# Performance work log

Hardware: AMD Instinct MI355X
Metric: run time of the kernel (lower is better)

The kernel has to match this reference:

```python
import jax, jax.numpy as jnp
import numpy as np

E, K = 16, 4          # n_experts, top_k
C, H = 2048, 3584     # d_model, ffn_hidden
B, T = 2, 512
STD = 0.02


def setup_inputs() -> dict:
    key = jax.random.key(0)
    ks = jax.random.split(key, 5)
    x = jax.random.normal(ks[0], (B, T, C), jnp.float32)
    W_up = jax.random.normal(ks[1], (E, H, C), jnp.float32) * STD
    W_gate = jax.random.normal(ks[2], (E, H, C), jnp.float32) * STD
    W_down = jax.random.normal(ks[3], (E, C, H), jnp.float32) * STD
    gate_inp = jax.random.normal(ks[4], (E, C), jnp.float32) * STD
    return {"x": x, "W_up": W_up, "W_gate": W_gate, "W_down": W_down,
            "gate_inp": gate_inp}


def reference(x, W_up, W_gate, W_down, gate_inp):
    # x: [B, T, C]
    b, t, c = x.shape
    xf = x.reshape(b * t, c)                                  # [N, C]
    logits = xf @ gate_inp.T                                  # [N, E]
    topv, topi = jax.lax.top_k(logits, K)                     # [N, K]
    w = jax.nn.softmax(topv.astype(jnp.float32), axis=-1).astype(x.dtype)
    n = xf.shape[0]
    # Dense combine weights: zero for unselected experts -> identical math
    # to the original per-token gather, without the [N,K,H,C] blowup.
    dense_w = jnp.zeros((n, E), x.dtype).at[jnp.arange(n)[:, None], topi].set(w)
    u = jnp.einsum('nc,ehc->neh', xf, W_up)                   # [N, E, H]
    g = jnp.einsum('nc,ehc->neh', xf, W_gate)                 # [N, E, H]
    h = jax.nn.silu(g) * u                                    # SwiGLU
    y = jnp.einsum('neh,ech,ne->nc', h, W_down, dense_w)      # weighted combine
    return y.reshape(b, t, c)
```

## Files before the change

kernel.cpp:

```cpp
#include <hip/hip_runtime.h>
#include <math.h>

#define NTOK   1024
#define EXP    16
#define TOPK   4
#define DMODEL 2048
#define DFFN   3584
#define HT_TILES 56
#define CT_TILES 32

typedef __attribute__((ext_vector_type(8))) short bf16x8;
typedef __attribute__((ext_vector_type(4))) float f32x4;

#define O_COUNTS 0
#define O_BASE   256
#define O_CURSOR 512
#define O_TOPI   4096
#define O_TOPW   (O_TOPI + 16384)
#define O_TOK    (O_TOPW + 16384)
#define O_WGT    (O_TOK + 16384)
#define O_SLOTNK (O_WGT + 16384)
#define O_HBUF   (O_SLOTNK + 16384)
#define O_YPART  (O_HBUF + (size_t)4096*DFFN*2)

__device__ __forceinline__ unsigned short f2b_rne(float f) {
  unsigned u = __builtin_bit_cast(unsigned, f);
  u += 0x7FFFu + ((u >> 16) & 1u);
  return (unsigned short)(u >> 16);
}
__device__ __forceinline__ float b2f(unsigned short h) {
  unsigned u = ((unsigned)h) << 16;
  return __builtin_bit_cast(float, u);
}

__device__ __forceinline__ void st_bf16x4(unsigned short* lds, int row, int c4, float4 v) {
  unsigned long long p = (unsigned long long)f2b_rne(v.x)
    | ((unsigned long long)f2b_rne(v.y) << 16)
    | ((unsigned long long)f2b_rne(v.z) << 32)
    | ((unsigned long long)f2b_rne(v.w) << 48);
  *(unsigned long long*)(lds + row*64 + (((c4 >> 1) ^ (row & 7)) * 8) + (c4 & 1) * 4) = p;
}
__device__ __forceinline__ bf16x8 ld_frag(const unsigned short* lds, int row, int chunk) {
  return *(const bf16x8*)(lds + row*64 + ((chunk ^ (row & 7)) * 8));
}

__global__ void k_zero(int* counts, int* cursor) {
  int t = threadIdx.x;
  if (t < EXP) { counts[t] = 0; cursor[t] = 0; }
}

__global__ void k_gate(const float* __restrict__ x, const float* __restrict__ gi,
                       int* __restrict__ topi, float* __restrict__ topw,
                       int* __restrict__ counts) {
  int n = blockIdx.x;
  int lane = threadIdx.x & 63, wave = threadIdx.x >> 6;
  __shared__ float lg[EXP];
  const float4* xr = (const float4*)(x + (size_t)n * DMODEL);
  #pragma unroll
  for (int i = 0; i < 4; ++i) {
    int e = wave * 4 + i;
    const float4* gr = (const float4*)(gi + (size_t)e * DMODEL);
    float s = 0.f;
    #pragma unroll
    for (int j = 0; j < 8; ++j) {
      float4 a = xr[j*64 + lane];
      float4 b = gr[j*64 + lane];
      s += a.x*b.x + a.y*b.y + a.z*b.z + a.w*b.w;
    }
    #pragma unroll
    for (int off = 32; off; off >>= 1) s += __shfl_xor(s, off);
    if (lane == 0) lg[e] = s;
  }
  __syncthreads();
  if (threadIdx.x == 0) {
    float v[EXP];
    #pragma unroll
    for (int j = 0; j < EXP; ++j) v[j] = lg[j];
    int bi[TOPK]; float bv[TOPK];
    #pragma unroll
    for (int k = 0; k < TOPK; ++k) {
      float best = -3.4e38f; int bidx = 0;
      for (int j = 0; j < EXP; ++j) if (v[j] > best) { best = v[j]; bidx = j; }
      bv[k] = best; bi[k] = bidx; v[bidx] = -3.4e38f;
    }
    float m = bv[0], ss = 0.f, w[TOPK];
    #pragma unroll
    for (int k = 0; k < TOPK; ++k) { w[k] = expf(bv[k] - m); ss += w[k]; }
    #pragma unroll
    for (int k = 0; k < TOPK; ++k) {
      topi[n*TOPK + k] = bi[k];
      topw[n*TOPK + k] = w[k] / ss;
      atomicAdd(&counts[bi[k]], 1);
    }
  }
}

__global__ void k_prefix(const int* __restrict__ counts, int* __restrict__ basep) {
  if (threadIdx.x == 0) {
    int acc = 0;
    for (int e = 0; e < EXP; ++e) { basep[e] = acc; acc += counts[e]; }
  }
}

__global__ void k_scatter(const int* __restrict__ topi, const float* __restrict__ topw,
                          const int* __restrict__ basep, int* __restrict__ cursor,
                          int* __restrict__ tok, float* __restrict__ wgt,
                          int* __restrict__ slotnk) {
  int n = blockIdx.x * blockDim.x + threadIdx.x;
  if (n >= NTOK) return;
  #pragma unroll
  for (int k = 0; k < TOPK; ++k) {
    int e = topi[n*TOPK + k];
    int pos = atomicAdd(&cursor[e], 1);
    int slot = basep[e] + pos;
    tok[slot] = n;
    wgt[slot] = topw[n*TOPK + k];
    slotnk[n*TOPK + k] = slot;
  }
}

__global__ __launch_bounds__(256) void k_upgate(
    const float* __restrict__ x, const float* __restrict__ Wu, const float* __restrict__ Wg,
    const int* __restrict__ counts, const int* __restrict__ basep,
    const int* __restrict__ tok, const float* __restrict__ wgt,
    unsigned short* __restrict__ hbuf) {
  int e  = blockIdx.x / HT_TILES;
  int ht = blockIdx.x % HT_TILES;
  int n_e = counts[e];
  if (n_e == 0) return;
  int base_e = basep[e];
  int nm = (n_e + 127) >> 7;

  __shared__ unsigned short xs[128*64];
  __shared__ unsigned short us[64*64];
  __shared__ unsigned short gs[64*64];
  __shared__ int   stok[128];
  __shared__ float swgt[128];

  int tid = threadIdx.x;
  int lane = tid & 63, wave = tid >> 6;
  int wm = wave >> 1, wh = wave & 1;
  const float* wu_base = Wu + ((size_t)e * DFFN + (size_t)ht * 64) * DMODEL;
  const float* wg_base = Wg + ((size_t)e * DFFN + (size_t)ht * 64) * DMODEL;

  for (int mch = 0; mch < nm; ++mch) {
    __syncthreads();
    if (tid < 128) {
      int r = mch*128 + tid;
      bool valid = r < n_e;
      stok[tid] = valid ? tok[base_e + r] : 0;
      swgt[tid] = valid ? wgt[base_e + r] : 0.f;
    }
    f32x4 ua[4][2], ga[4][2];
    #pragma unroll
    for (int t = 0; t < 4; ++t)
      #pragma unroll
      for (int j = 0; j < 2; ++j) {
        f32x4 z = {0.f, 0.f, 0.f, 0.f};
        ua[t][j] = z; ga[t][j] = z;
      }

    for (int kc = 0; kc < DMODEL/64; ++kc) {
      __syncthreads();
      #pragma unroll
      for (int i = 0; i < 8; ++i) {
        int idx = i*256 + tid;
        int row = idx >> 4, c4 = idx & 15;
        float4 v = *(const float4*)(x + (size_t)stok[row]*DMODEL + kc*64 + c4*4);
        st_bf16x4(xs, row, c4, v);
      }
      #pragma unroll
      for (int i = 0; i < 4; ++i) {
        int idx = i*256 + tid;
        int row = idx >> 4, c4 = idx & 15;
        st_bf16x4(us, row, c4, *(const float4*)(wu_base + (size_t)row*DMODEL + kc*64 + c4*4));
        st_bf16x4(gs, row, c4, *(const float4*)(wg_base + (size_t)row*DMODEL + kc*64 + c4*4));
      }
      __syncthreads();
      #pragma unroll
      for (int kk = 0; kk < 2; ++kk) {
        int chunk = kk*4 + (lane >> 4);
        bf16x8 a[4], bu[2], bg[2];
        #pragma unroll
        for (int t = 0; t < 4; ++t) a[t] = ld_frag(xs, wm*64 + t*16 + (lane & 15), chunk);
        #pragma unroll
        for (int j = 0; j < 2; ++j) {
          bu[j] = ld_frag(us, wh*32 + j*16 + (lane & 15), chunk);
          bg[j] = ld_frag(gs, wh*32 + j*16 + (lane & 15), chunk);
        }
        #pragma unroll
        for (int t = 0; t < 4; ++t)
          #pragma unroll
          for (int j = 0; j < 2; ++j) {
            ua[t][j] = __builtin_amdgcn_mfma_f32_16x16x32_bf16(a[t], bu[j], ua[t][j], 0, 0, 0);
            ga[t][j] = __builtin_amdgcn_mfma_f32_16x16x32_bf16(a[t], bg[j], ga[t][j], 0, 0, 0);
          }
      }
    }
    #pragma unroll
    for (int t = 0; t < 4; ++t)
      #pragma unroll
      for (int j = 0; j < 2; ++j)
        #pragma unroll
        for (int r = 0; r < 4; ++r) {
          int ml = wm*64 + t*16 + (lane >> 4)*4 + r;
          if (mch*128 + ml < n_e) {
            float u = ua[t][j][r], g = ga[t][j][r];
            float hv = u * (g / (1.f + expf(-g))) * swgt[ml];
            int slot = base_e + mch*128 + ml;
            hbuf[(size_t)slot*DFFN + ht*64 + wh*32 + j*16 + (lane & 15)] = f2b_rne(hv);
          }
        }
  }
}

__global__ __launch_bounds__(256) void k_down(
    const unsigned short* __restrict__ hbuf, const float* __restrict__ Wd,
    const int* __restrict__ counts, const int* __restrict__ basep,
    unsigned short* __restrict__ ypart) {
  int e  = blockIdx.x / CT_TILES;
  int ct = blockIdx.x % CT_TILES;
  int n_e = counts[e];
  if (n_e == 0) return;
  int base_e = basep[e];
  int nm = (n_e + 127) >> 7;

  __shared__ unsigned short hs[128*64];
  __shared__ unsigned short dw[64*64];

  int tid = threadIdx.x;
  int lane = tid & 63, wave = tid >> 6;
  int wm = wave >> 1, wh = wave & 1;
  const float* wd_base = Wd + ((size_t)e * DMODEL + (size_t)ct * 64) * DFFN;

  for (int mch = 0; mch < nm; ++mch) {
    f32x4 acc[4][2];
    #pragma unroll
    for (int t = 0; t < 4; ++t)
      #pragma unroll
      for (int j = 0; j < 2; ++j) { f32x4 z = {0.f,0.f,0.f,0.f}; acc[t][j] = z; }

    for (int hc = 0; hc < DFFN/64; ++hc) {
      __syncthreads();
      #pragma unroll
      for (int i = 0; i < 4; ++i) {
        int idx = i*256 + tid;
        int row = idx >> 3, c8 = idx & 7;
        int slot = base_e + mch*128 + row;
        if (slot > 4095) slot = 4095;
        uint4 v = *(const uint4*)(hbuf + (size_t)slot*DFFN + hc*64 + c8*8);
        *(uint4*)(hs + row*64 + ((c8 ^ (row & 7)) * 8)) = v;
      }
      #pragma unroll
      for (int i = 0; i < 4; ++i) {
        int idx = i*256 + tid;
        int row = idx >> 4, c4 = idx & 15;
        st_bf16x4(dw, row, c4, *(const float4*)(wd_base + (size_t)row*DFFN + hc*64 + c4*4));
      }
      __syncthreads();
      #pragma unroll
      for (int kk = 0; kk < 2; ++kk) {
        int chunk = kk*4 + (lane >> 4);
        bf16x8 a[4], b[2];
        #pragma unroll
        for (int t = 0; t < 4; ++t) a[t] = ld_frag(hs, wm*64 + t*16 + (lane & 15), chunk);
        #pragma unroll
        for (int j = 0; j < 2; ++j) b[j] = ld_frag(dw, wh*32 + j*16 + (lane & 15), chunk);
        #pragma unroll
        for (int t = 0; t < 4; ++t)
          #pragma unroll
          for (int j = 0; j < 2; ++j)
            acc[t][j] = __builtin_amdgcn_mfma_f32_16x16x32_bf16(a[t], b[j], acc[t][j], 0, 0, 0);
      }
    }
    #pragma unroll
    for (int t = 0; t < 4; ++t)
      #pragma unroll
      for (int j = 0; j < 2; ++j)
        #pragma unroll
        for (int r = 0; r < 4; ++r) {
          int ml = wm*64 + t*16 + (lane >> 4)*4 + r;
          if (mch*128 + ml < n_e) {
            int slot = base_e + mch*128 + ml;
            ypart[(size_t)slot*DMODEL + ct*64 + wh*32 + j*16 + (lane & 15)] =
                f2b_rne(acc[t][j][r]);
          }
        }
  }
}

__global__ void k_combine(const unsigned short* __restrict__ ypart,
                          const int* __restrict__ slotnk, float* __restrict__ out) {
  int n = blockIdx.x, tid = threadIdx.x;
  int c0 = tid * 8;
  float acc[8] = {0.f,0.f,0.f,0.f,0.f,0.f,0.f,0.f};
  #pragma unroll
  for (int k = 0; k < TOPK; ++k) {
    int slot = slotnk[n*TOPK + k];
    uint4 v = *(const uint4*)(ypart + (size_t)slot*DMODEL + c0);
    const unsigned short* p = (const unsigned short*)&v;
    #pragma unroll
    for (int j = 0; j < 8; ++j) acc[j] += b2f(p[j]);
  }
  float4 o0 = {acc[0], acc[1], acc[2], acc[3]};
  float4 o1 = {acc[4], acc[5], acc[6], acc[7]};
  *(float4*)(out + (size_t)n*DMODEL + c0)     = o0;
  *(float4*)(out + (size_t)n*DMODEL + c0 + 4) = o1;
}

extern "C" void kernel_launch(void* const* d_in, const int* in_sizes, int n_in,
                              void* d_out, int out_size, void* d_ws, size_t ws_size,
                              hipStream_t stream) {
  const float* x     = (const float*)d_in[0];
  const float* W_up  = (const float*)d_in[1];
  const float* W_gt  = (const float*)d_in[2];
  const float* W_dn  = (const float*)d_in[3];
  const float* g_in  = (const float*)d_in[4];
  float* out = (float*)d_out;
  char* ws = (char*)d_ws;

  int*   counts = (int*)(ws + O_COUNTS);
  int*   basep  = (int*)(ws + O_BASE);
  int*   cursor = (int*)(ws + O_CURSOR);
  int*   topi   = (int*)(ws + O_TOPI);
  float* topw   = (float*)(ws + O_TOPW);
  int*   tok    = (int*)(ws + O_TOK);
  float* wgt    = (float*)(ws + O_WGT);
  int*   slotnk = (int*)(ws + O_SLOTNK);
  unsigned short* hbuf  = (unsigned short*)(ws + O_HBUF);
  unsigned short* ypart = (unsigned short*)(ws + O_YPART);

  k_zero   <<<1, 64, 0, stream>>>(counts, cursor);
  k_gate   <<<NTOK, 256, 0, stream>>>(x, g_in, topi, topw, counts);
  k_prefix <<<1, 64, 0, stream>>>(counts, basep);
  k_scatter<<<4, 256, 0, stream>>>(topi, topw, basep, cursor, tok, wgt, slotnk);
  k_upgate <<<EXP*HT_TILES, 256, 0, stream>>>(x, W_up, W_gt, counts, basep, tok, wgt, hbuf);
  k_down   <<<EXP*CT_TILES, 256, 0, stream>>>(hbuf, W_dn, counts, basep, ypart);
  k_combine<<<NTOK, 256, 0, stream>>>(ypart, slotnk, out);
}
```

Baseline: 881.6 us.

## Pre-gather bf16 tokens and double-buffer LDS with async global-to-LDS loads

```diff
diff --git a/kernel.cpp b/kernel.cpp
--- a/kernel.cpp
+++ b/kernel.cpp
@@ -8,6 +8,7 @@
 #define DFFN   3584
 #define HT_TILES 56
 #define CT_TILES 32
+#define NSLOT  4096
 
 typedef __attribute__((ext_vector_type(8))) short bf16x8;
 typedef __attribute__((ext_vector_type(4))) float f32x4;
@@ -20,8 +21,8 @@
 #define O_TOK    (O_TOPW + 16384)
 #define O_WGT    (O_TOK + 16384)
 #define O_SLOTNK (O_WGT + 16384)
-#define O_HBUF   (O_SLOTNK + 16384)
-#define O_YPART  (O_HBUF + (size_t)4096*DFFN*2)
+#define O_XG     (O_SLOTNK + 16384)
+#define O_HBUF   (O_XG + (size_t)NSLOT*DMODEL*2)
 
 __device__ __forceinline__ unsigned short f2b_rne(float f) {
   unsigned u = __builtin_bit_cast(unsigned, f);
@@ -31,6 +32,12 @@
 __device__ __forceinline__ float b2f(unsigned short h) {
   unsigned u = ((unsigned)h) << 16;
   return __builtin_bit_cast(float, u);
+}
+
+__device__ __forceinline__ void gl16(const unsigned short* g, unsigned short* l) {
+  __builtin_amdgcn_global_load_lds(
+      (const __attribute__((address_space(1))) void*)g,
+      (__attribute__((address_space(3))) void*)l, 16, 0, 0);
 }
 
 __device__ __forceinline__ void st_bf16x4(unsigned short* lds, int row, int c4, float4 v) {
@@ -119,10 +126,27 @@
   }
 }
 
+__global__ void k_gather(const float* __restrict__ x, const int* __restrict__ tok,
+                         unsigned short* __restrict__ xg) {
+  int slot = blockIdx.x;
+  int t = tok[slot];
+  int c0 = threadIdx.x * 8;
+  const float* src = x + (size_t)t * DMODEL + c0;
+  float4 a = *(const float4*)(src);
+  float4 b = *(const float4*)(src + 4);
+  unsigned u0 = (unsigned)f2b_rne(a.x) | ((unsigned)f2b_rne(a.y) << 16);
+  unsigned u1 = (unsigned)f2b_rne(a.z) | ((unsigned)f2b_rne(a.w) << 16);
+  unsigned u2 = (unsigned)f2b_rne(b.x) | ((unsigned)f2b_rne(b.y) << 16);
+  unsigned u3 = (unsigned)f2b_rne(b.z) | ((unsigned)f2b_rne(b.w) << 16);
+  uint4 o = {u0, u1, u2, u3};
+  *(uint4*)(xg + (size_t)slot * DMODEL + c0) = o;
+}
+
 __global__ __launch_bounds__(256) void k_upgate(
-    const float* __restrict__ x, const float* __restrict__ Wu, const float* __restrict__ Wg,
+    const unsigned short* __restrict__ xg,
+    const float* __restrict__ Wu, const float* __restrict__ Wg,
     const int* __restrict__ counts, const int* __restrict__ basep,
-    const int* __restrict__ tok, const float* __restrict__ wgt,
+    const float* __restrict__ wgt,
     unsigned short* __restrict__ hbuf) {
   int e  = blockIdx.x / HT_TILES;
   int ht = blockIdx.x % HT_TILES;
@@ -131,10 +155,9 @@
   int base_e = basep[e];
   int nm = (n_e + 127) >> 7;
 
-  __shared__ unsigned short xs[128*64];
-  __shared__ unsigned short us[64*64];
-  __shared__ unsigned short gs[64*64];
-  __shared__ int   stok[128];
+  __shared__ unsigned short xs[2][128*64];
+  __shared__ unsigned short us[2][64*64];
+  __shared__ unsigned short gs[2][64*64];
   __shared__ float swgt[128];
 
   int tid = threadIdx.x;
@@ -143,50 +166,79 @@
   const float* wu_base = Wu + ((size_t)e * DFFN + (size_t)ht * 64) * DMODEL;
   const float* wg_base = Wg + ((size_t)e * DFFN + (size_t)ht * 64) * DMODEL;
 
+  int xrow_lo = lane >> 3;
+  int xpc     = lane & 7;
+
+  float4 wur[4], wgr[4];
+
   for (int mch = 0; mch < nm; ++mch) {
     __syncthreads();
     if (tid < 128) {
       int r = mch*128 + tid;
-      bool valid = r < n_e;
-      stok[tid] = valid ? tok[base_e + r] : 0;
-      swgt[tid] = valid ? wgt[base_e + r] : 0.f;
-    }
+      swgt[tid] = (r < n_e) ? wgt[base_e + r] : 0.f;
+    }
+
+    #pragma unroll
+    for (int i = 0; i < 4; ++i) {
+      int row = (i*4 + wave)*8 + xrow_lo;
+      int slotr = base_e + mch*128 + row;
+      if (slotr > NSLOT-1) slotr = NSLOT-1;
+      const unsigned short* src = xg + (size_t)slotr*DMODEL + ((xpc ^ (row & 7)) * 8);
+      gl16(src, &xs[0][(i*4 + wave)*8*64]);
+    }
+    #pragma unroll
+    for (int i = 0; i < 4; ++i) {
+      int idx = i*256 + tid, row = idx >> 4, c4 = idx & 15;
+      wur[i] = *(const float4*)(wu_base + (size_t)row*DMODEL + c4*4);
+      wgr[i] = *(const float4*)(wg_base + (size_t)row*DMODEL + c4*4);
+    }
+    #pragma unroll
+    for (int i = 0; i < 4; ++i) {
+      int idx = i*256 + tid, row = idx >> 4, c4 = idx & 15;
+      st_bf16x4(us[0], row, c4, wur[i]);
+      st_bf16x4(gs[0], row, c4, wgr[i]);
+    }
+    __syncthreads();
+
     f32x4 ua[4][2], ga[4][2];
     #pragma unroll
     for (int t = 0; t < 4; ++t)
       #pragma unroll
       for (int j = 0; j < 2; ++j) {
-        f32x4 z = {0.f, 0.f, 0.f, 0.f};
+        f32x4 z = {0.f,0.f,0.f,0.f};
         ua[t][j] = z; ga[t][j] = z;
       }
 
     for (int kc = 0; kc < DMODEL/64; ++kc) {
-      __syncthreads();
-      #pragma unroll
-      for (int i = 0; i < 8; ++i) {
-        int idx = i*256 + tid;
-        int row = idx >> 4, c4 = idx & 15;
-        float4 v = *(const float4*)(x + (size_t)stok[row]*DMODEL + kc*64 + c4*4);
-        st_bf16x4(xs, row, c4, v);
-      }
-      #pragma unroll
-      for (int i = 0; i < 4; ++i) {
-        int idx = i*256 + tid;
-        int row = idx >> 4, c4 = idx & 15;
-        st_bf16x4(us, row, c4, *(const float4*)(wu_base + (size_t)row*DMODEL + kc*64 + c4*4));
-        st_bf16x4(gs, row, c4, *(const float4*)(wg_base + (size_t)row*DMODEL + kc*64 + c4*4));
-      }
-      __syncthreads();
+      const int cur = kc & 1, nxt = cur ^ 1;
+      const bool pf = (kc + 1 < DMODEL/64);
+      if (pf) {
+        #pragma unroll
+        for (int i = 0; i < 4; ++i) {
+          int row = (i*4 + wave)*8 + xrow_lo;
+          int slotr = base_e + mch*128 + row;
+          if (slotr > NSLOT-1) slotr = NSLOT-1;
+          const unsigned short* src = xg + (size_t)slotr*DMODEL + (kc+1)*64
+                                         + ((xpc ^ (row & 7)) * 8);
+          gl16(src, &xs[nxt][(i*4 + wave)*8*64]);
+        }
+        #pragma unroll
+        for (int i = 0; i < 4; ++i) {
+          int idx = i*256 + tid, row = idx >> 4, c4 = idx & 15;
+          wur[i] = *(const float4*)(wu_base + (size_t)row*DMODEL + (kc+1)*64 + c4*4);
+          wgr[i] = *(const float4*)(wg_base + (size_t)row*DMODEL + (kc+1)*64 + c4*4);
+        }
+      }
       #pragma unroll
       for (int kk = 0; kk < 2; ++kk) {
         int chunk = kk*4 + (lane >> 4);
         bf16x8 a[4], bu[2], bg[2];
         #pragma unroll
-        for (int t = 0; t < 4; ++t) a[t] = ld_frag(xs, wm*64 + t*16 + (lane & 15), chunk);
+        for (int t = 0; t < 4; ++t) a[t] = ld_frag(xs[cur], wm*64 + t*16 + (lane & 15), chunk);
         #pragma unroll
         for (int j = 0; j < 2; ++j) {
-          bu[j] = ld_frag(us, wh*32 + j*16 + (lane & 15), chunk);
-          bg[j] = ld_frag(gs, wh*32 + j*16 + (lane & 15), chunk);
+          bu[j] = ld_frag(us[cur], wh*32 + j*16 + (lane & 15), chunk);
+          bg[j] = ld_frag(gs[cur], wh*32 + j*16 + (lane & 15), chunk);
         }
         #pragma unroll
         for (int t = 0; t < 4; ++t)
@@ -196,7 +248,17 @@
             ga[t][j] = __builtin_amdgcn_mfma_f32_16x16x32_bf16(a[t], bg[j], ga[t][j], 0, 0, 0);
           }
       }
-    }
+      if (pf) {
+        #pragma unroll
+        for (int i = 0; i < 4; ++i) {
+          int idx = i*256 + tid, row = idx >> 4, c4 = idx & 15;
+          st_bf16x4(us[nxt], row, c4, wur[i]);
+          st_bf16x4(gs[nxt], row, c4, wgr[i]);
+        }
+      }
+      __syncthreads();
+    }
+
     #pragma unroll
     for (int t = 0; t < 4; ++t)
       #pragma unroll
@@ -225,15 +287,41 @@
   int base_e = basep[e];
   int nm = (n_e + 127) >> 7;
 
-  __shared__ unsigned short hs[128*64];
-  __shared__ unsigned short dw[64*64];
+  __shared__ unsigned short hs[2][128*64];
+  __shared__ unsigned short dwS[2][64*64];
 
   int tid = threadIdx.x;
   int lane = tid & 63, wave = tid >> 6;
   int wm = wave >> 1, wh = wave & 1;
   const float* wd_base = Wd + ((size_t)e * DMODEL + (size_t)ct * 64) * DFFN;
 
+  int xrow_lo = lane >> 3;
+  int xpc     = lane & 7;
+
+  float4 wdr[4];
+
   for (int mch = 0; mch < nm; ++mch) {
+    __syncthreads();
+    #pragma unroll
+    for (int i = 0; i < 4; ++i) {
+      int row = (i*4 + wave)*8 + xrow_lo;
+      int slotr = base_e + mch*128 + row;
+      if (slotr > NSLOT-1) slotr = NSLOT-1;
+      const unsigned short* src = hbuf + (size_t)slotr*DFFN + ((xpc ^ (row & 7)) * 8);
+      gl16(src, &hs[0][(i*4 + wave)*8*64]);
+    }
+    #pragma unroll
+    for (int i = 0; i < 4; ++i) {
+      int idx = i*256 + tid, row = idx >> 4, c4 = idx & 15;
+      wdr[i] = *(const float4*)(wd_base + (size_t)row*DFFN + c4*4);
+    }
+    #pragma unroll
+    for (int i = 0; i < 4; ++i) {
+      int idx = i*256 + tid, row = idx >> 4, c4 = idx & 15;
+      st_bf16x4(dwS[0], row, c4, wdr[i]);
+    }
+    __syncthreads();
+
     f32x4 acc[4][2];
     #pragma unroll
     for (int t = 0; t < 4; ++t)
@@ -241,38 +329,48 @@
       for (int j = 0; j < 2; ++j) { f32x4 z = {0.f,0.f,0.f,0.f}; acc[t][j] = z; }
 
     for (int hc = 0; hc < DFFN/64; ++hc) {
-      __syncthreads();
-      #pragma unroll
-      for (int i = 0; i < 4; ++i) {
-        int idx = i*256 + tid;
-        int row = idx >> 3, c8 = idx & 7;
-        int slot = base_e + mch*128 + row;
-        if (slot > 4095) slot = 4095;
-        uint4 v = *(const uint4*)(hbuf + (size_t)slot*DFFN + hc*64 + c8*8);
-        *(uint4*)(hs + row*64 + ((c8 ^ (row & 7)) * 8)) = v;
-      }
-      #pragma unroll
-      for (int i = 0; i < 4; ++i) {
-        int idx = i*256 + tid;
-        int row = idx >> 4, c4 = idx & 15;
-        st_bf16x4(dw, row, c4, *(const float4*)(wd_base + (size_t)row*DFFN + hc*64 + c4*4));
-      }
-      __syncthreads();
+      const int cur = hc & 1, nxt = cur ^ 1;
+      const bool pf = (hc + 1 < DFFN/64);
+      if (pf) {
+        #pragma unroll
+        for (int i = 0; i < 4; ++i) {
+          int row = (i*4 + wave)*8 + xrow_lo;
+          int slotr = base_e + mch*128 + row;
+          if (slotr > NSLOT-1) slotr = NSLOT-1;
+          const unsigned short* src = hbuf + (size_t)slotr*DFFN + (hc+1)*64
+                                          + ((xpc ^ (row & 7)) * 8);
+          gl16(src, &hs[nxt][(i*4 + wave)*8*64]);
+        }
+        #pragma unroll
+        for (int i = 0; i < 4; ++i) {
+          int idx = i*256 + tid, row = idx >> 4, c4 = idx & 15;
+          wdr[i] = *(const float4*)(wd_base + (size_t)row*DFFN + (hc+1)*64 + c4*4);
+        }
+      }
       #pragma unroll
       for (int kk = 0; kk < 2; ++kk) {
         int chunk = kk*4 + (lane >> 4);
         bf16x8 a[4], b[2];
         #pragma unroll
-        for (int t = 0; t < 4; ++t) a[t] = ld_frag(hs, wm*64 + t*16 + (lane & 15), chunk);
-        #pragma unroll
-        for (int j = 0; j < 2; ++j) b[j] = ld_frag(dw, wh*32 + j*16 + (lane & 15), chunk);
+        for (int t = 0; t < 4; ++t) a[t] = ld_frag(hs[cur], wm*64 + t*16 + (lane & 15), chunk);
+        #pragma unroll
+        for (int j = 0; j < 2; ++j) b[j] = ld_frag(dwS[cur], wh*32 + j*16 + (lane & 15), chunk);
         #pragma unroll
         for (int t = 0; t < 4; ++t)
           #pragma unroll
           for (int j = 0; j < 2; ++j)
             acc[t][j] = __builtin_amdgcn_mfma_f32_16x16x32_bf16(a[t], b[j], acc[t][j], 0, 0, 0);
       }
-    }
+      if (pf) {
+        #pragma unroll
+        for (int i = 0; i < 4; ++i) {
+          int idx = i*256 + tid, row = idx >> 4, c4 = idx & 15;
+          st_bf16x4(dwS[nxt], row, c4, wdr[i]);
+        }
+      }
+      __syncthreads();
+    }
+
     #pragma unroll
     for (int t = 0; t < 4; ++t)
       #pragma unroll
@@ -327,14 +425,16 @@
   int*   tok    = (int*)(ws + O_TOK);
   float* wgt    = (float*)(ws + O_WGT);
   int*   slotnk = (int*)(ws + O_SLOTNK);
+  unsigned short* xg    = (unsigned short*)(ws + O_XG);
   unsigned short* hbuf  = (unsigned short*)(ws + O_HBUF);
-  unsigned short* ypart = (unsigned short*)(ws + O_YPART);
+  unsigned short* ypart = xg;
 
   k_zero   <<<1, 64, 0, stream>>>(counts, cursor);
   k_gate   <<<NTOK, 256, 0, stream>>>(x, g_in, topi, topw, counts);
   k_prefix <<<1, 64, 0, stream>>>(counts, basep);
   k_scatter<<<4, 256, 0, stream>>>(topi, topw, basep, cursor, tok, wgt, slotnk);
-  k_upgate <<<EXP*HT_TILES, 256, 0, stream>>>(x, W_up, W_gt, counts, basep, tok, wgt, hbuf);
+  k_gather <<<NSLOT, 256, 0, stream>>>(x, tok, xg);
+  k_upgate <<<EXP*HT_TILES, 256, 0, stream>>>(xg, W_up, W_gt, counts, basep, wgt, hbuf);
   k_down   <<<EXP*CT_TILES, 256, 0, stream>>>(hbuf, W_dn, counts, basep, ypart);
   k_combine<<<NTOK, 256, 0, stream>>>(ypart, slotnk, out);
 }
```

Result: slower. 1.134 ms (+28.7%).
